# Performance work log

Measured on AMD Instinct MI355X. Metric: run time of the kernel, lower is better.

## Reference

```python
import jax, jax.numpy as jnp
import numpy as np

B, NIN, NREG, D, H, L = 8, 1024, 16, 1024, 16, 12
DFF = 4 * D
S = NIN + NREG
HD = D // H
EPS = 1e-6


def setup_inputs() -> dict:
    key = jax.random.key(0)
    ks = jax.random.split(key, 8)
    p = lambda k, shape: jax.random.normal(k, shape, jnp.float32) * 0.02
    return dict(
        x=jax.random.normal(ks[0], (B, S, D), jnp.float32),
        n_input=NIN,
        ln1_g=jnp.ones((L, D), jnp.float32), ln1_b=jnp.zeros((L, D), jnp.float32),
        wqkv=p(ks[1], (L, D, 3 * D)), bqkv=jnp.zeros((L, 3 * D), jnp.float32),
        wo=p(ks[2], (L, D, D)), bo=jnp.zeros((L, D), jnp.float32),
        ln2_g=jnp.ones((L, D), jnp.float32), ln2_b=jnp.zeros((L, D), jnp.float32),
        w1=p(ks[3], (L, D, DFF)), b1=jnp.zeros((L, DFF), jnp.float32),
        w2=p(ks[4], (L, DFF, D)), b2=jnp.zeros((L, D), jnp.float32),
        lnf_g=jnp.ones((D,), jnp.float32), lnf_b=jnp.zeros((D,), jnp.float32),
    )


def _ln(x, g, b):
    mu = x.mean(-1, keepdims=True)
    var = ((x - mu) ** 2).mean(-1, keepdims=True)
    return (x - mu) * jax.lax.rsqrt(var + EPS) * g + b


def _build_mask(n_input, total):
    # inputs attend everywhere; registers attend to all inputs and causally among registers
    i = jnp.arange(total)[:, None]
    j = jnp.arange(total)[None, :]
    blocked = (i >= n_input) & (j >= n_input) & (j > i)
    return jnp.where(blocked, -jnp.inf, 0.0).astype(jnp.float32)  # (S, S) additive


def _attn(h, wqkv_l, bqkv_l, wo_l, bo_l, mask):
    b, s, _ = h.shape
    qkv = h @ wqkv_l + bqkv_l                                   # (B,S,3D)
    q, k, v = jnp.split(qkv, 3, axis=-1)
    q = q.reshape(b, s, H, HD).transpose(0, 2, 1, 3)            # (B,H,S,HD)
    k = k.reshape(b, s, H, HD).transpose(0, 2, 1, 3)
    v = v.reshape(b, s, H, HD).transpose(0, 2, 1, 3)
    scores = jnp.einsum('bhqd,bhkd->bhqk', q, k) / np.sqrt(HD) + mask
    a = jax.nn.softmax(scores, axis=-1)
    o = jnp.einsum('bhqk,bhkd->bhqd', a, v)
    o = o.transpose(0, 2, 1, 3).reshape(b, s, D)
    return o @ wo_l + bo_l


def reference(x, n_input, ln1_g, ln1_b, wqkv, bqkv, wo, bo,
              ln2_g, ln2_b, w1, b1, w2, b2, lnf_g, lnf_b):
    mask = _build_mask(n_input, x.shape[1])

    def blk(h, p):
        l1g, l1b, wq, bq, wo_, bo_, l2g, l2b, w1_, b1_, w2_, b2_ = p
        h = h + _attn(_ln(h, l1g, l1b), wq, bq, wo_, bo_, mask)
        u = _ln(h, l2g, l2b) @ w1_ + b1_
        h = h + jax.nn.gelu(u) @ w2_ + b2_
        return h, None

    h, _ = jax.lax.scan(blk, x, (ln1_g, ln1_b, wqkv, bqkv, wo, bo,
                                 ln2_g, ln2_b, w1, b1, w2, b2))
    return _ln(h, lnf_g, lnf_b)
```

## Files before the change

### kernel.cpp

```cpp
#include <hip/hip_runtime.h>
#include <hip/hip_bf16.h>
#include <stdint.h>

#define DD   1024
#define TD   3072
#define DFFN 4096
#define NL   12
#define SS   1040
#define SP   1056
#define BB   8
#define MM   (BB*SS)
#define HH   16
#define NTAIL 32

typedef float  f32x4  __attribute__((ext_vector_type(4)));
typedef __bf16 bf16x8 __attribute__((ext_vector_type(8)));
typedef unsigned short u16;

union Bf8 { bf16x8 v; u16 s[8]; };

__device__ __forceinline__ u16 f2b(float f) {
  union { float f; unsigned u; } x; x.f = f;
  unsigned r = (x.u + 0x7FFFu + ((x.u >> 16) & 1u)) >> 16;
  return (u16)r;
}

__device__ __forceinline__ f32x4 mfma_bf16(bf16x8 a, bf16x8 b, f32x4 c) {
  return __builtin_amdgcn_mfma_f32_16x16x32_bf16(a, b, c, 0, 0, 0);
}

__device__ __forceinline__ void gload_lds16(const u16* g, u16* l) {
  __builtin_amdgcn_global_load_lds((const __attribute__((address_space(1))) void*)g,
                                   (__attribute__((address_space(3))) void*)l, 16, 0, 0);
}

__device__ __forceinline__ float dppmax16(float t) {
  union { float f; int i; } u, v;
  u.f = t;
  v.i = __builtin_amdgcn_update_dpp(0, u.i, 0xB1, 0xF, 0xF, true);
  u.f = fmaxf(u.f, v.f);
  v.i = __builtin_amdgcn_update_dpp(0, u.i, 0x4E, 0xF, 0xF, true);
  u.f = fmaxf(u.f, v.f);
  v.i = __builtin_amdgcn_update_dpp(0, u.i, 0x124, 0xF, 0xF, true);
  u.f = fmaxf(u.f, v.f);
  v.i = __builtin_amdgcn_update_dpp(0, u.i, 0x128, 0xF, 0xF, true);
  u.f = fmaxf(u.f, v.f);
  return u.f;
}

__global__ __launch_bounds__(256)
void transpose_cast(const float* __restrict__ in, u16* __restrict__ out, int K, int N) {
  __shared__ float tile[32][33];
  const int n0 = blockIdx.x * 32, k0 = blockIdx.y * 32;
  const size_t lb = (size_t)blockIdx.z * K * N;
  const int tx = threadIdx.x, ty = threadIdx.y;
  for (int j = 0; j < 4; ++j)
    tile[ty + 8*j][tx] = in[lb + (size_t)(k0 + ty + 8*j) * N + n0 + tx];
  __syncthreads();
  for (int j = 0; j < 4; ++j)
    out[lb + (size_t)(n0 + ty + 8*j) * K + k0 + tx] = f2b(tile[tx][ty + 8*j]);
}

template<int OUTF>
__global__ __launch_bounds__(256)
void ln_kernel(const float* __restrict__ in, const float* __restrict__ gam,
               const float* __restrict__ bet, u16* __restrict__ outb, float* __restrict__ outf) {
  const int row = blockIdx.x, t = threadIdx.x;
  const float4 v = ((const float4*)(in + (size_t)row * DD))[t];
  float s  = v.x + v.y + v.z + v.w;
  float s2 = v.x*v.x + v.y*v.y + v.z*v.z + v.w*v.w;
  for (int off = 1; off < 64; off <<= 1) { s += __shfl_xor(s, off); s2 += __shfl_xor(s2, off); }
  __shared__ float red[8];
  if ((t & 63) == 0) { red[t >> 6] = s; red[4 + (t >> 6)] = s2; }
  __syncthreads();
  s  = red[0] + red[1] + red[2] + red[3];
  s2 = red[4] + red[5] + red[6] + red[7];
  const float mu = s * (1.0f/1024.0f);
  const float var = s2 * (1.0f/1024.0f) - mu*mu;
  const float rs = rsqrtf(var + 1e-6f);
  const float4 gv = ((const float4*)gam)[t];
  const float4 bv = ((const float4*)bet)[t];
  const float y0 = (v.x - mu)*rs*gv.x + bv.x;
  const float y1 = (v.y - mu)*rs*gv.y + bv.y;
  const float y2 = (v.z - mu)*rs*gv.z + bv.z;
  const float y3 = (v.w - mu)*rs*gv.w + bv.w;
  if (OUTF) {
    float4 o; o.x=y0; o.y=y1; o.z=y2; o.w=y3;
    ((float4*)(outf + (size_t)row * DD))[t] = o;
  } else {
    ushort4 o; o.x=f2b(y0); o.y=f2b(y1); o.z=f2b(y2); o.w=f2b(y3);
    ((ushort4*)(outb + (size_t)row * DD))[t] = o;
  }
}

template<int EPI>
__global__ __launch_bounds__(256, 4)
void gemm_bt(const u16* __restrict__ A, const u16* __restrict__ Bt,
             const float* __restrict__ bias, const float* __restrict__ resid,
             float* outF, u16* outB,
             u16* __restrict__ qb, u16* __restrict__ kb, u16* __restrict__ vtb,
             int N, int K) {
  __shared__ u16 As[128*64];
  __shared__ u16 Bs[128*64];
  const int tid = threadIdx.x;

  const int nwg = gridDim.x * gridDim.y;
  int wgid = blockIdx.y * gridDim.x + blockIdx.x;
  wgid = (wgid & 7) * (nwg >> 3) + (wgid >> 3);
  const int nb = wgid % gridDim.y;
  const int mb = wgid / gridDim.y;
  const int m0 = mb * 128, n0 = nb * 128;

  const int lane = tid & 63, w = tid >> 6;
  const int wr = (w >> 1) * 64, wc = (w & 1) * 64;
  const int c = lane & 15, g = lane >> 4;

  f32x4 acc[4][4];
  for (int i = 0; i < 4; ++i) for (int j = 0; j < 4; ++j) acc[i][j] = f32x4{0.f,0.f,0.f,0.f};

  const int srow = tid >> 3, scg = tid & 7;
  const size_t aoff = (size_t)(m0 + srow) * K + scg * 8;
  const size_t boff = (size_t)(n0 + srow) * K + scg * 8;

  for (int kt = 0; kt < K; kt += 64) {
    for (int it = 0; it < 4; ++it) {
      gload_lds16(A  + aoff + (size_t)it * 32 * K + kt, As + (it*256 + tid) * 8);
      gload_lds16(Bt + boff + (size_t)it * 32 * K + kt, Bs + (it*256 + tid) * 8);
    }
    __syncthreads();
    for (int kk = 0; kk < 2; ++kk) {
      bf16x8 af[4], bfr[4];
      for (int i = 0; i < 4; ++i) af[i]  = *(const bf16x8*)(As + (wr + i*16 + c)*64 + kk*32 + g*8);
      for (int j = 0; j < 4; ++j) bfr[j] = *(const bf16x8*)(Bs + (wc + j*16 + c)*64 + kk*32 + g*8);
      for (int i = 0; i < 4; ++i)
        for (int j = 0; j < 4; ++j)
          acc[i][j] = mfma_bf16(af[i], bfr[j], acc[i][j]);
    }
    __syncthreads();
  }

  for (int j = 0; j < 4; ++j) {
    const int col = n0 + wc + j*16 + c;
    const float bcol = bias[col];
    for (int i = 0; i < 4; ++i) {
      const int row0 = m0 + wr + i*16 + 4*g;
      if (EPI == 3) {
        const int part = col >> 10;
        const int hh2  = (col >> 6) & 15;
        const int hd   = col & 63;
        const int bb   = (int)((unsigned)row0 / SS);
        const int s0   = row0 - bb * SS;
        const size_t bh = (size_t)(bb * HH + hh2);
        if (part == 2) {
          ushort4 pk;
          pk.x = f2b(acc[i][j][0] + bcol);
          pk.y = f2b(acc[i][j][1] + bcol);
          pk.z = f2b(acc[i][j][2] + bcol);
          pk.w = f2b(acc[i][j][3] + bcol);
          *(ushort4*)(vtb + (bh*64 + hd)*SP + s0) = pk;
        } else if (part == 0) {
          for (int r = 0; r < 4; ++r)
            qb[(bh*SP + s0 + r)*64 + hd] = f2b((acc[i][j][r] + bcol) * 0.125f);
        } else {
          for (int r = 0; r < 4; ++r)
            kb[(bh*SP + s0 + r)*64 + hd] = f2b(acc[i][j][r] + bcol);
        }
      } else {
        for (int r = 0; r < 4; ++r) {
          const size_t idx = (size_t)(row0 + r) * N + col;
          const float v = acc[i][j][r] + bcol;
          if (EPI == 1) {
            const float z = 1.5957691216f * (v + 0.044715f * v * v * v);
            const float e = __expf(z);
            outB[idx] = f2b(v * e * __builtin_amdgcn_rcpf(e + 1.0f));
          } else {
            outF[idx] = v + resid[idx];
          }
        }
      }
    }
  }
}

__global__ __launch_bounds__(256, 4)
void gemm64(const u16* __restrict__ A, const u16* __restrict__ Bt,
            const float* __restrict__ bias, const float* __restrict__ resid,
            float* __restrict__ outF, int N, int K) {
  __shared__ u16 As[64*64];
  __shared__ u16 Bs[128*64];
  const int tid = threadIdx.x;

  const int nwg = gridDim.x * gridDim.y;
  int wgid = blockIdx.y * gridDim.x + blockIdx.x;
  wgid = (wgid & 7) * (nwg >> 3) + (wgid >> 3);
  const int nb = wgid % gridDim.y;
  const int mb = wgid / gridDim.y;
  const int m0 = mb * 64, n0 = nb * 128;

  const int lane = tid & 63, w = tid >> 6;
  const int wr = (w >> 1) * 32, wc = (w & 1) * 64;
  const int c = lane & 15, g = lane >> 4;

  f32x4 acc[2][4];
  for (int i = 0; i < 2; ++i) for (int j = 0; j < 4; ++j) acc[i][j] = f32x4{0.f,0.f,0.f,0.f};

  const int srow = tid >> 3, scg = tid & 7;
  const size_t aoff = (size_t)(m0 + srow) * K + scg * 8;
  const size_t boff = (size_t)(n0 + srow) * K + scg * 8;

  for (int kt = 0; kt < K; kt += 64) {
    for (int it = 0; it < 2; ++it)
      gload_lds16(A  + aoff + (size_t)it * 32 * K + kt, As + (it*256 + tid) * 8);
    for (int it = 0; it < 4; ++it)
      gload_lds16(Bt + boff + (size_t)it * 32 * K + kt, Bs + (it*256 + tid) * 8);
    __syncthreads();
    for (int kk = 0; kk < 2; ++kk) {
      bf16x8 af[2], bfr[4];
      for (int i = 0; i < 2; ++i) af[i]  = *(const bf16x8*)(As + (wr + i*16 + c)*64 + kk*32 + g*8);
      for (int j = 0; j < 4; ++j) bfr[j] = *(const bf16x8*)(Bs + (wc + j*16 + c)*64 + kk*32 + g*8);
      for (int i = 0; i < 2; ++i)
        for (int j = 0; j < 4; ++j)
          acc[i][j] = mfma_bf16(af[i], bfr[j], acc[i][j]);
    }
    __syncthreads();
  }

  for (int j = 0; j < 4; ++j) {
    const int col = n0 + wc + j*16 + c;
    const float bcol = bias[col];
    for (int i = 0; i < 2; ++i) {
      const int row0 = m0 + wr + i*16 + 4*g;
      for (int r = 0; r < 4; ++r) {
        const size_t idx = (size_t)(row0 + r) * N + col;
        outF[idx] = acc[i][j][r] + bcol + resid[idx];
      }
    }
  }
}

__global__ __launch_bounds__(256, 4)
void attn_staged(const u16* __restrict__ Qb, const u16* __restrict__ Kb,
                 const u16* __restrict__ VTb, u16* __restrict__ out,
                 const int* __restrict__ npt) {
  __shared__ u16 KV[2][4096];
  __shared__ u16 PT[4][640];
  const int tid = threadIdx.x;
  const int w = tid >> 6, lane = tid & 63;
  const int c = lane & 15, g = lane >> 4;
  const int nin = npt[0];
  u16* pw = PT[w];

  if (blockIdx.x < NTAIL) {
    const int bh = blockIdx.x * 4 + w;
    const int b = bh >> 4, hh = bh & 15;
    const int q0 = 64 * 16;

    bf16x8 aq0, aq1;
    {
      const u16* qp = Qb + ((size_t)bh * SP + q0 + c) * 64 + g * 8;
      aq0 = *(const bf16x8*)qp;
      aq1 = *(const bf16x8*)(qp + 32);
    }

    float m[4], ls[4];
    f32x4 o[4];
    int qrow[4];
    for (int r = 0; r < 4; ++r) { m[r] = -1e30f; ls[r] = 0.f; qrow[r] = q0 + 4*g + r; }
    for (int nd = 0; nd < 4; ++nd) o[nd] = f32x4{0.f,0.f,0.f,0.f};

    for (int kt = 0; kt < 33; ++kt) {
      const int k0 = kt * 32;

      f32x4 s[2];
      {
        const u16* kp0 = Kb + ((size_t)bh * SP + k0 + c) * 64 + g * 8;
        f32x4 z0 = f32x4{0.f,0.f,0.f,0.f};
        z0 = mfma_bf16(aq0, *(const bf16x8*)kp0, z0);
        z0 = mfma_bf16(aq1, *(const bf16x8*)(kp0 + 32), z0);
        s[0] = z0;
        const u16* kp1 = kp0 + 16 * 64;
        f32x4 z1 = f32x4{0.f,0.f,0.f,0.f};
        z1 = mfma_bf16(aq0, *(const bf16x8*)kp1, z1);
        z1 = mfma_bf16(aq1, *(const bf16x8*)(kp1 + 32), z1);
        s[1] = z1;
      }

      for (int jt = 0; jt < 2; ++jt) {
        const int j = k0 + jt*16 + c;
        for (int r = 0; r < 4; ++r) {
          const int q = qrow[r];
          const bool blocked = (j >= SS) || ((q >= nin) && (j >= nin) && (j > q));
          if (blocked) s[jt][r] = -1e30f;
        }
      }

      for (int r = 0; r < 4; ++r) {
        float t = fmaxf(s[0][r], s[1][r]);
        for (int off = 1; off < 16; off <<= 1) t = fmaxf(t, __shfl_xor(t, off));
        const float mn = fmaxf(m[r], t);
        const float al = __expf(m[r] - mn);
        m[r] = mn;
        const float p0 = __expf(s[0][r] - mn);
        const float p1 = __expf(s[1][r] - mn);
        s[0][r] = p0; s[1][r] = p1;
        float ps = p0 + p1;
        for (int off = 1; off < 16; off <<= 1) ps += __shfl_xor(ps, off);
        ls[r] = ls[r] * al + ps;
        for (int nd = 0; nd < 4; ++nd) o[nd][r] *= al;
      }

      for (int jt = 0; jt < 2; ++jt)
        for (int r = 0; r < 4; ++r)
          pw[(4*g + r)*40 + jt*16 + c] = f2b(s[jt][r]);
      __builtin_amdgcn_sched_barrier(0);
      bf16x8 ap = *(const bf16x8*)(pw + c*40 + 8*g);
      __builtin_amdgcn_sched_barrier(0);

      for (int nd = 0; nd < 4; ++nd) {
        const u16* vp = VTb + ((size_t)bh * 64 + nd*16 + c) * SP + k0 + 8*g;
        o[nd] = mfma_bf16(ap, *(const bf16x8*)vp, o[nd]);
      }
    }

    for (int nd = 0; nd < 4; ++nd)
      for (int r = 0; r < 4; ++r) {
        const float v = o[nd][r] / ls[r];
        out[((size_t)b * SS + qrow[r]) * DD + hh*64 + nd*16 + c] = f2b(v);
      }
    return;
  }

  const int sb = blockIdx.x - NTAIL;
  const int bh = sb & 127;
  const int qg = sb >> 7;
  const int b = bh >> 4, hh = bh & 15;

  const u16 *ssrc0, *ssrc1; int kstr; u16 *sdst0, *sdst1;
  if (tid < 128) {
    const int i0 = tid, i1 = tid + 128;
    const int r0 = i0 >> 3, cg0 = (i0 & 7) ^ (r0 & 7);
    const int r1 = i1 >> 3, cg1 = (i1 & 7) ^ (r1 & 7);
    ssrc0 = Kb + ((size_t)bh * SP + r0) * 64 + cg0 * 8;
    ssrc1 = Kb + ((size_t)bh * SP + r1) * 64 + cg1 * 8;
    kstr = 32 * 64;
    sdst0 = &KV[0][i0 * 8];
    sdst1 = &KV[0][i1 * 8];
  } else {
    const int t2 = tid - 128;
    const int i0 = t2, i1 = t2 + 128;
    const int r0 = i0 >> 2, cg0 = (i0 & 3) ^ (r0 & 3);
    const int r1 = i1 >> 2, cg1 = (i1 & 3) ^ (r1 & 3);
    ssrc0 = VTb + ((size_t)bh * 64 + r0) * SP + cg0 * 8;
    ssrc1 = VTb + ((size_t)bh * 64 + r1) * SP + cg1 * 8;
    kstr = 32;
    sdst0 = &KV[0][2048 + i0 * 8];
    sdst1 = &KV[0][2048 + i1 * 8];
  }
#define STAGE(bufbit, kt) do { \
    gload_lds16(ssrc0 + (size_t)(kt) * kstr, sdst0 + (bufbit) * 4096); \
    gload_lds16(ssrc1 + (size_t)(kt) * kstr, sdst1 + (bufbit) * 4096); } while (0)

  bf16x8 aq[2][2];
  int q0[2];
#pragma unroll
  for (int qq = 0; qq < 2; ++qq) {
    q0[qq] = (qg * 8 + w * 2 + qq) * 16;
    const u16* qp = Qb + ((size_t)bh * SP + q0[qq] + c) * 64 + g * 8;
    aq[qq][0] = *(const bf16x8*)qp;
    aq[qq][1] = *(const bf16x8*)(qp + 32);
  }

  Bf8 onesf;
  for (int i = 0; i < 8; ++i) onesf.s[i] = (c == 0) ? (u16)0x3F80 : (u16)0;

  float m[2][4];
  f32x4 o[2][5];
#pragma unroll
  for (int qq = 0; qq < 2; ++qq) {
    for (int r = 0; r < 4; ++r) m[qq][r] = -1e30f;
    for (int nd = 0; nd < 5; ++nd) o[qq][nd] = f32x4{0.f,0.f,0.f,0.f};
  }
  const bool tregs0 = (q0[0] + 15) >= nin;
  const bool tregs1 = (q0[1] + 15) >= nin;
  const int c7 = c & 7, c3 = c & 3;

  STAGE(0, 0);

  for (int kt = 0; kt < 33; ++kt) {
    const int buf = kt & 1;
    __syncthreads();
    if (kt < 32) STAGE(buf ^ 1, kt + 1);
    const u16* Kt = &KV[buf][0];
    const u16* Vt = &KV[buf][2048];
    const int k0 = kt * 32;

    bf16x8 k00 = *(const bf16x8*)(Kt + c*64        + ((g    ) ^ c7) * 8);
    bf16x8 k01 = *(const bf16x8*)(Kt + c*64        + ((g + 4) ^ c7) * 8);
    bf16x8 k10 = *(const bf16x8*)(Kt + (c+16)*64   + ((g    ) ^ c7) * 8);
    bf16x8 k11 = *(const bf16x8*)(Kt + (c+16)*64   + ((g + 4) ^ c7) * 8);

#pragma unroll
    for (int qq = 0; qq < 2; ++qq) {
      f32x4 s[2];
      {
        f32x4 z0 = f32x4{0.f,0.f,0.f,0.f};
        z0 = mfma_bf16(aq[qq][0], k00, z0);
        z0 = mfma_bf16(aq[qq][1], k01, z0);
        s[0] = z0;
        f32x4 z1 = f32x4{0.f,0.f,0.f,0.f};
        z1 = mfma_bf16(aq[qq][0], k10, z1);
        z1 = mfma_bf16(aq[qq][1], k11, z1);
        s[1] = z1;
      }

      const bool tregs = qq ? tregs1 : tregs0;
      if (tregs || (k0 + 31 >= SS)) {
        const int qr0 = q0[qq] + 4*g;
        for (int jt = 0; jt < 2; ++jt) {
          const int j = k0 + jt*16 + c;
          for (int r = 0; r < 4; ++r) {
            const int q = qr0 + r;
            const bool blocked = (j >= SS) || ((q >= nin) && (j >= nin) && (j > q));
            if (blocked) s[jt][r] = -1e30f;
          }
        }
      }

      for (int r = 0; r < 4; ++r) {
        const float t = dppmax16(fmaxf(s[0][r], s[1][r]));
        const float mn = fmaxf(m[qq][r], t);
        const float al = __expf(m[qq][r] - mn);
        m[qq][r] = mn;
        for (int nd = 0; nd < 5; ++nd) o[qq][nd][r] *= al;
        s[0][r] = __expf(s[0][r] - mn);
        s[1][r] = __expf(s[1][r] - mn);
      }

      for (int jt = 0; jt < 2; ++jt)
        for (int r = 0; r < 4; ++r)
          pw[(4*g + r)*40 + jt*16 + c] = f2b(s[jt][r]);
      __builtin_amdgcn_sched_barrier(0);
      bf16x8 ap = *(const bf16x8*)(pw + c*40 + 8*g);
      __builtin_amdgcn_sched_barrier(0);

      for (int nd = 0; nd < 4; ++nd) {
        bf16x8 bv = *(const bf16x8*)(Vt + (nd*16 + c)*32 + ((g ^ c3) * 8));
        o[qq][nd] = mfma_bf16(ap, bv, o[qq][nd]);
      }
      o[qq][4] = mfma_bf16(ap, onesf.v, o[qq][4]);
    }
  }
#undef STAGE

#pragma unroll
  for (int qq = 0; qq < 2; ++qq) {
    float rls[4];
    for (int r = 0; r < 4; ++r)
      rls[r] = 1.0f / __shfl(o[qq][4][r], lane & 48);
    const int qr0 = q0[qq] + 4*g;
    for (int nd = 0; nd < 4; ++nd)
      for (int r = 0; r < 4; ++r)
        out[((size_t)b * SS + qr0 + r) * DD + hh*64 + nd*16 + c] = f2b(o[qq][nd][r] * rls[r]);
  }
}

extern "C" void kernel_launch(void* const* d_in, const int* in_sizes, int n_in,
                              void* d_out, int out_size, void* d_ws, size_t ws_size,
                              hipStream_t stream) {
  const float* x    = (const float*)d_in[0];
  const int*   npt  = (const int*)  d_in[1];
  const float* ln1g = (const float*)d_in[2];
  const float* ln1b = (const float*)d_in[3];
  const float* wqkv = (const float*)d_in[4];
  const float* bqkv = (const float*)d_in[5];
  const float* wo   = (const float*)d_in[6];
  const float* bo   = (const float*)d_in[7];
  const float* ln2g = (const float*)d_in[8];
  const float* ln2b = (const float*)d_in[9];
  const float* w1   = (const float*)d_in[10];
  const float* b1   = (const float*)d_in[11];
  const float* w2   = (const float*)d_in[12];
  const float* b2   = (const float*)d_in[13];
  const float* lnfg = (const float*)d_in[14];
  const float* lnfb = (const float*)d_in[15];

  char* ws = (char*)d_ws;
  size_t off = 0;
  u16*   wqkvT = (u16*)(ws + off);   off += (size_t)NL*TD*DD*2;
  u16*   woT   = (u16*)(ws + off);   off += (size_t)NL*DD*DD*2;
  u16*   w1T   = (u16*)(ws + off);   off += (size_t)NL*DFFN*DD*2;
  u16*   w2T   = (u16*)(ws + off);   off += (size_t)NL*DD*DFFN*2;
  float* h     = (float*)(ws + off); off += (size_t)MM*DD*4;
  u16*   lnb   = (u16*)(ws + off);   off += (size_t)MM*DD*2;
  u16*   Qb    = (u16*)(ws + off);   off += (size_t)BB*HH*SP*64*2;
  u16*   Kb    = (u16*)(ws + off);   off += (size_t)BB*HH*SP*64*2;
  u16*   VTb   = (u16*)(ws + off);   off += (size_t)BB*HH*64*SP*2;
  u16*   attnO = (u16*)(ws + off);   off += (size_t)MM*DD*2;
  u16*   ffh   = (u16*)(ws + off);   off += (size_t)MM*DFFN*2;

  const dim3 tb(32, 8);
  transpose_cast<<<dim3(TD/32,   DD/32,   NL), tb, 0, stream>>>(wqkv, wqkvT, DD,   TD);
  transpose_cast<<<dim3(DD/32,   DD/32,   NL), tb, 0, stream>>>(wo,   woT,   DD,   DD);
  transpose_cast<<<dim3(DFFN/32, DD/32,   NL), tb, 0, stream>>>(w1,   w1T,   DD,   DFFN);
  transpose_cast<<<dim3(DD/32,   DFFN/32, NL), tb, 0, stream>>>(w2,   w2T,   DFFN, DD);
  hipMemcpyAsync(h, x, (size_t)MM*DD*4, hipMemcpyDeviceToDevice, stream);
  hipMemsetAsync(Qb, 0, (size_t)3*BB*HH*SP*64*2, stream);

  for (int l = 0; l < NL; ++l) {
    ln_kernel<0><<<MM, 256, 0, stream>>>(h, ln1g + (size_t)l*DD, ln1b + (size_t)l*DD, lnb, nullptr);
    gemm_bt<3><<<dim3(MM/128, TD/128), 256, 0, stream>>>(
        lnb, wqkvT + (size_t)l*TD*DD, bqkv + (size_t)l*TD, nullptr, nullptr, nullptr,
        Qb, Kb, VTb, TD, DD);
    attn_staged<<<dim3(1024 + NTAIL), 256, 0, stream>>>(Qb, Kb, VTb, attnO, npt);
    gemm64<<<dim3(MM/64, DD/128), 256, 0, stream>>>(
        attnO, woT + (size_t)l*DD*DD, bo + (size_t)l*DD, h, h, DD, DD);
    ln_kernel<0><<<MM, 256, 0, stream>>>(h, ln2g + (size_t)l*DD, ln2b + (size_t)l*DD, lnb, nullptr);
    gemm_bt<1><<<dim3(MM/128, DFFN/128), 256, 0, stream>>>(
        lnb, w1T + (size_t)l*DFFN*DD, b1 + (size_t)l*DFFN, nullptr, nullptr, ffh,
        nullptr, nullptr, nullptr, DFFN, DD);
    gemm_bt<2><<<dim3(MM/128, DD/128), 256, 0, stream>>>(
        ffh, w2T + (size_t)l*DD*DFFN, b2 + (size_t)l*DD, h, h, nullptr,
        nullptr, nullptr, nullptr, DD, DFFN);
  }
  ln_kernel<1><<<MM, 256, 0, stream>>>(h, lnfg, lnfb, nullptr, (float*)d_out);
}
```

Baseline: 5.730 ms.

## Split K across two wave groups in the FFN down-projection GEMM

Adds a 512-thread GEMM kernel for the FFN down-projection. Two groups of four waves each cover half of the K=4096 reduction for the same 128x128 tile and reduce partial sums through LDS before applying bias and the residual. The goal is more waves per output tile, to hide memory latency in a GEMM with a small grid (65x8 workgroups) and a long K. The cost is more LDS per workgroup (64KB), a shared-memory reduction step, and possibly lower occupancy.

```diff
diff --git a/kernel.cpp b/kernel.cpp
--- a/kernel.cpp
+++ b/kernel.cpp
@@ -182,6 +182,82 @@
   }
 }
 
+__global__ __launch_bounds__(512, 2)
+void gemm_splitk(const u16* __restrict__ A, const u16* __restrict__ Bt,
+                 const float* __restrict__ bias, const float* __restrict__ resid,
+                 float* __restrict__ outF, int N, int K) {
+  __shared__ u16 smem[4 * 128 * 64];
+  const int tid = threadIdx.x;
+  const int gg = tid >> 8;
+  const int t2 = tid & 255;
+
+  u16* As = smem + gg * (128*64);
+  u16* Bs = smem + 2*(128*64) + gg * (128*64);
+
+  const int nwg = gridDim.x * gridDim.y;
+  int wgid = blockIdx.y * gridDim.x + blockIdx.x;
+  wgid = (wgid & 7) * (nwg >> 3) + (wgid >> 3);
+  const int nb = wgid % gridDim.y;
+  const int mb = wgid / gridDim.y;
+  const int m0 = mb * 128, n0 = nb * 128;
+
+  const int lane = tid & 63, w = (tid >> 6) & 3;
+  const int wr = (w >> 1) * 64, wc = (w & 1) * 64;
+  const int c = lane & 15, g = lane >> 4;
+
+  f32x4 acc[4][4];
+  for (int i = 0; i < 4; ++i) for (int j = 0; j < 4; ++j) acc[i][j] = f32x4{0.f,0.f,0.f,0.f};
+
+  const int srow = t2 >> 3, scg = t2 & 7;
+  const int kbase = gg * (K >> 1);
+  const size_t aoff = (size_t)(m0 + srow) * K + scg * 8 + kbase;
+  const size_t boff = (size_t)(n0 + srow) * K + scg * 8 + kbase;
+
+  const int KH = K >> 1;
+  for (int kt = 0; kt < KH; kt += 64) {
+    for (int it = 0; it < 4; ++it) {
+      gload_lds16(A  + aoff + (size_t)it * 32 * K + kt, As + (it*256 + t2) * 8);
+      gload_lds16(Bt + boff + (size_t)it * 32 * K + kt, Bs + (it*256 + t2) * 8);
+    }
+    __syncthreads();
+    for (int kk = 0; kk < 2; ++kk) {
+      bf16x8 af[4], bfr[4];
+      for (int i = 0; i < 4; ++i) af[i]  = *(const bf16x8*)(As + (wr + i*16 + c)*64 + kk*32 + g*8);
+      for (int j = 0; j < 4; ++j) bfr[j] = *(const bf16x8*)(Bs + (wc + j*16 + c)*64 + kk*32 + g*8);
+      for (int i = 0; i < 4; ++i)
+        for (int j = 0; j < 4; ++j)
+          acc[i][j] = mfma_bf16(af[i], bfr[j], acc[i][j]);
+    }
+    __syncthreads();
+  }
+
+  f32x4* Red = (f32x4*)smem;
+  if (gg == 1) {
+#pragma unroll
+    for (int k = 0; k < 16; ++k)
+      Red[k * 256 + t2] = acc[k >> 2][k & 3];
+  }
+  __syncthreads();
+  if (gg == 0) {
+#pragma unroll
+    for (int k = 0; k < 16; ++k) {
+      const f32x4 v = Red[k * 256 + t2];
+      acc[k >> 2][k & 3] += v;
+    }
+    for (int j = 0; j < 4; ++j) {
+      const int col = n0 + wc + j*16 + c;
+      const float bcol = bias[col];
+      for (int i = 0; i < 4; ++i) {
+        const int row0 = m0 + wr + i*16 + 4*g;
+        for (int r = 0; r < 4; ++r) {
+          const size_t idx = (size_t)(row0 + r) * N + col;
+          outF[idx] = acc[i][j][r] + bcol + resid[idx];
+        }
+      }
+    }
+  }
+}
+
 __global__ __launch_bounds__(256, 4)
 void gemm64(const u16* __restrict__ A, const u16* __restrict__ Bt,
             const float* __restrict__ bias, const float* __restrict__ resid,
@@ -518,9 +594,8 @@
     gemm_bt<1><<<dim3(MM/128, DFFN/128), 256, 0, stream>>>(
         lnb, w1T + (size_t)l*DFFN*DD, b1 + (size_t)l*DFFN, nullptr, nullptr, ffh,
         nullptr, nullptr, nullptr, DFFN, DD);
-    gemm_bt<2><<<dim3(MM/128, DD/128), 256, 0, stream>>>(
-        ffh, w2T + (size_t)l*DD*DFFN, b2 + (size_t)l*DD, h, h, nullptr,
-        nullptr, nullptr, nullptr, DD, DFFN);
+    gemm_splitk<<<dim3(MM/128, DD/128), 512, 0, stream>>>(
+        ffh, w2T + (size_t)l*DD*DFFN, b2 + (size_t)l*DD, h, h, DD, DFFN);
   }
   ln_kernel<1><<<MM, 256, 0, stream>>>(h, lnfg, lnfb, nullptr, (float*)d_out);
 }
```

Result: slower. 6.729 ms (+17.4%).
